# Kernel tuning notes

Hardware: AMD Instinct MI355X
Metric: run time of the kernel (lower is better)

Reference implementation:

```python
import jax, jax.numpy as jnp
import numpy as np

INV_TEMP = 20.0
THRESHOLD = 0.01
SING_CUTOFF = 3.0
D0 = 128  # order-0 descriptor block
EPS = 1e-6


def setup_inputs() -> dict:
    key = jax.random.key(0)
    ks = jax.random.split(key, 6)
    B, N, M, D = 4, 4096, 4096, 256
    K = (D - D0) // 2
    return {
        "keypoints_A": jax.random.uniform(ks[0], (B, N, 2), jnp.float32) * 2.0 - 1.0,
        "descriptions_A": jax.random.normal(ks[1], (B, N, D), jnp.float32),
        "keypoints_B": jax.random.uniform(ks[2], (B, M, 2), jnp.float32) * 2.0 - 1.0,
        "descriptions_B": jax.random.normal(ks[3], (B, M, D), jnp.float32),
        "W_lstsq": jax.random.normal(ks[4], (D0, K), jnp.float32) * 0.1,
        "b_lstsq": jnp.zeros((K,), jnp.float32),
    }


def _svdvals_2x2(A):
    # singular values of [..,2,2] via eigenvalues of A^T A (closed form)
    M = jnp.einsum('...ki,...kj->...ij', A, A)
    t = M[..., 0, 0] + M[..., 1, 1]
    d = M[..., 0, 0] * M[..., 1, 1] - M[..., 0, 1] * M[..., 1, 0]
    disc = jnp.sqrt(jnp.maximum(0.25 * t * t - d, 0.0))
    lam_hi = 0.5 * t + disc
    lam_lo = jnp.maximum(0.5 * t - disc, 0.0)
    return jnp.sqrt(lam_hi), jnp.sqrt(lam_lo)


def reference(keypoints_A, descriptions_A, keypoints_B, descriptions_B, W_lstsq, b_lstsq):
    B, N, D = descriptions_A.shape
    K = (D - D0) // 2
    # --- dual softmax matcher (normalize=True) ---
    dA = descriptions_A / jnp.linalg.norm(descriptions_A, axis=-1, keepdims=True)
    dB = descriptions_B / jnp.linalg.norm(descriptions_B, axis=-1, keepdims=True)
    sim = INV_TEMP * jnp.einsum('bnd,bmd->bnm', dA, dB)  # [B,N,M]
    P = jax.nn.softmax(sim, axis=-2) * jax.nn.softmax(sim, axis=-1)
    # --- mutual nearest neighbors, fixed-shape (one candidate per A-row) ---
    j = jnp.argmax(P, axis=-1)  # [B,N]
    Pij = jnp.take_along_axis(P, j[..., None], axis=-1)[..., 0]
    colmax_j = jnp.take_along_axis(P.max(axis=-2), j, axis=-1)
    valid = (Pij >= colmax_j) & (Pij > THRESHOLD)  # mutual max + threshold
    # --- gather raw descriptors for matched pairs ---
    descB_m = jnp.take_along_axis(descriptions_B, j[..., None], axis=1)  # [B,N,D]
    desc0_A, desc1_A = descriptions_A[..., :D0], descriptions_A[..., D0:]
    desc0_B, desc1_B = descB_m[..., :D0], descB_m[..., D0:]
    # --- lstsq weights from order-0 features ---
    wA = jax.nn.softplus(desc0_A @ W_lstsq + b_lstsq)
    wB = jax.nn.softplus(desc0_B @ W_lstsq + b_lstsq)
    w = jnp.sqrt(wA * wB)  # [B,N,K]
    # --- weighted 2x2 affine lstsq: A x ~ y ---
    X = desc1_A.reshape(B, N, K, 2)
    Y = desc1_B.reshape(B, N, K, 2)
    G = jnp.einsum('bnk,bnki,bnkj->bnij', w, X, X) + EPS * jnp.eye(2, dtype=X.dtype)
    C = jnp.einsum('bnk,bnki,bnkj->bnij', w, Y, X)
    est = jnp.swapaxes(jnp.linalg.solve(G, jnp.swapaxes(C, -1, -2)), -1, -2)  # [B,N,2,2]
    # --- singular value / determinant filter ---
    s_hi, s_lo = _svdvals_2x2(est)
    good = jnp.isfinite(s_hi + s_lo) & (s_hi < SING_CUTOFF) & (s_lo > 1.0 / SING_CUTOFF)
    det = est[..., 0, 0] * est[..., 1, 1] - est[..., 0, 1] * est[..., 1, 0]
    good = good & (det > 0)  # remove_negative_determinants=True
    valid = valid & good
    matches_A = keypoints_A  # row i of A pairs with column j[b,i]
    matches_B = jnp.take_along_axis(keypoints_B, j[..., None], axis=1)
    return matches_A, matches_B, j, valid
```

## Files before the change

kernel.cpp:

```cpp
#include <hip/hip_runtime.h>
#include <math.h>

#define Bb   4
#define Nn   4096
#define Mm   4096
#define Dd   256
#define D0c  128
#define Kc   64

typedef _Float16 half8 __attribute__((ext_vector_type(8)));
typedef float    f32x4 __attribute__((ext_vector_type(4)));

__device__ __forceinline__ unsigned encf(float f) {
    unsigned u = __float_as_uint(f);
    return (u & 0x80000000u) ? ~u : (u | 0x80000000u);
}
__device__ __forceinline__ float decf(unsigned u) {
    return (u & 0x80000000u) ? __uint_as_float(u ^ 0x80000000u) : __uint_as_float(~u);
}
__device__ __forceinline__ float softplusf(float x) {
    return fmaxf(x, 0.f) + log1pf(expf(-fabsf(x)));
}
__device__ __forceinline__ void gl_lds16(const _Float16* g, _Float16* l) {
    __builtin_amdgcn_global_load_lds((const __attribute__((address_space(1))) void*)g,
                                     (__attribute__((address_space(3))) void*)l, 16, 0, 0);
}

__device__ __forceinline__ void decode_tile(int bid, int swz, int& mt, int& nt, int& zz) {
    if (swz == 2) {
        const int xcd = bid & 7, k = bid >> 3;
        zz = xcd >> 2;
        const int s = xcd & 3;
        mt = (s & 1) * 16 + (k & 15);
        nt = (s >> 1) * 16 + (k >> 4);
    } else if (swz == 1) {
        const int xcd = bid & 7, k = bid >> 3;
        zz = 0;
        const int s = xcd >> 1;
        const int t = (xcd & 1) * 128 + k;
        mt = (s & 1) * 16 + (t & 15);
        nt = (s >> 1) * 16 + (t >> 4);
    } else {
        mt = bid & 31; nt = (bid >> 5) & 31; zz = bid >> 10;
    }
}

__global__ __launch_bounds__(256) void prep_kernel(
    const float* __restrict__ dA, const float* __restrict__ dB,
    _Float16* __restrict__ Ah, _Float16* __restrict__ Al,
    _Float16* __restrict__ Bh, _Float16* __restrict__ Bl,
    unsigned* __restrict__ colMaxU)
{
    const int t = threadIdx.x, wave = t >> 6, lane = t & 63;
    const int row = blockIdx.x * 4 + wave;
    if (blockIdx.y == 0 && lane == 0) colMaxU[row] = 0u;
    const float* src = blockIdx.y ? dB : dA;
    _Float16* dh = blockIdx.y ? Bh : Ah;
    _Float16* dl = blockIdx.y ? Bl : Al;
    const float4 v = *(const float4*)&src[(size_t)row * Dd + lane * 4];
    float ss = v.x * v.x + v.y * v.y + v.z * v.z + v.w * v.w;
#pragma unroll
    for (int m = 32; m; m >>= 1) ss += __shfl_xor(ss, m, 64);
    const float inv = 1.0f / sqrtf(ss);
    float x[4] = {v.x * inv, v.y * inv, v.z * inv, v.w * inv};
    union { _Float16 h[4]; uint2 u; } ph, pl;
#pragma unroll
    for (int i = 0; i < 4; i++) {
        _Float16 h = (_Float16)x[i];
        ph.h[i] = h;
        pl.h[i] = (_Float16)((x[i] - (float)h) * 4096.f);
    }
    const size_t toff = (size_t)(row >> 7) * 32768
                      + (size_t)(lane >> 3) * 4096
                      + (size_t)((lane >> 1) & 3) * 1024
                      + (size_t)(row & 127) * 8 + (lane & 1) * 4;
    *(uint2*)&dh[toff] = ph.u;
    *(uint2*)&dl[toff] = pl.u;
}

template<int PB, int STORE>
__global__ __launch_bounds__(256, 2) void sim_kernel(
    const _Float16* __restrict__ Ah, const _Float16* __restrict__ Al,
    const _Float16* __restrict__ Bh, const _Float16* __restrict__ Bl,
    const float* __restrict__ Lrow_g, const float* __restrict__ Lcol_g,
    float* __restrict__ rowsumP, float* __restrict__ colsumP,
    float* __restrict__ rkey, int* __restrict__ rmArr, float* __restrict__ rcvArr,
    unsigned* __restrict__ cmU, float* __restrict__ simG, int b0, int swz)
{
    __shared__ _Float16 lds[2][4][4][128][8];
    __shared__ float    colp[128];
    __shared__ unsigned colu[128];
    __shared__ float    shL[128], shLc[128];

    const int t = threadIdx.x;
    const int wave = t >> 6, lane = t & 63;
    int mt, nt, bbl;
    decode_tile(blockIdx.x, swz, mt, nt, bbl);
    const int bb = b0 + bbl;
    const int n0 = nt * 128, m0 = mt * 128;

    if (PB) {
        if (t < 128) {
            shL[t]  = Lrow_g[bb * Nn + n0 + t];
            shLc[t] = Lcol_g[bb * Mm + m0 + t];
            colu[t] = 0u;
        }
    } else {
        if (t < 128) colp[t] = 0.f;
    }

    const _Float16* gb;
    {
        const size_t offA = (size_t)(bb * Nn + n0) * Dd;
        const size_t offB = (size_t)(bb * Mm + m0) * Dd;
        if      (wave == 0) gb = Ah + offA;
        else if (wave == 1) gb = Al + offA;
        else if (wave == 2) gb = Bh + offB;
        else                gb = Bl + offB;
    }

    f32x4 acc1[2][8], acc2[2][8];
#pragma unroll
    for (int ti = 0; ti < 2; ti++)
#pragma unroll
        for (int tj = 0; tj < 8; tj++) { acc1[ti][tj] = (f32x4)0.f; acc2[ti][tj] = (f32x4)0.f; }

    const int quad = lane >> 4, l15 = lane & 15;
    _Float16* lw0 = &lds[0][wave][0][0][0];
    _Float16* lw1 = &lds[1][wave][0][0][0];

#pragma unroll
    for (int q = 0; q < 8; ++q)
        gl_lds16(gb + q * 512 + lane * 8, lw0 + q * 512);

#pragma unroll
    for (int kc8 = 0; kc8 < 8; ++kc8) {
        const int cur = kc8 & 1;
        if (kc8 < 7) {
            _Float16* nw = cur ? lw0 : lw1;
            const _Float16* gsrc = gb + (kc8 + 1) * 4096;
#pragma unroll
            for (int q = 0; q < 8; ++q)
                gl_lds16(gsrc + q * 512 + lane * 8, nw + q * 512);
            asm volatile("s_waitcnt vmcnt(8)" ::: "memory");
        } else {
            asm volatile("s_waitcnt vmcnt(0)" ::: "memory");
        }
        __builtin_amdgcn_s_barrier();
        __builtin_amdgcn_sched_barrier(0);

        half8 afh[2], afl[2];
        afh[0] = *(const half8*)&lds[cur][0][quad][wave * 32 + l15][0];
        afh[1] = *(const half8*)&lds[cur][0][quad][wave * 32 + 16 + l15][0];
        afl[0] = *(const half8*)&lds[cur][1][quad][wave * 32 + l15][0];
        afl[1] = *(const half8*)&lds[cur][1][quad][wave * 32 + 16 + l15][0];
#pragma unroll
        for (int tj = 0; tj < 8; ++tj) {
            half8 bh = *(const half8*)&lds[cur][2][quad][tj * 16 + l15][0];
            half8 bl = *(const half8*)&lds[cur][3][quad][tj * 16 + l15][0];
#pragma unroll
            for (int ti = 0; ti < 2; ++ti) {
                acc1[ti][tj] = __builtin_amdgcn_mfma_f32_16x16x32_f16(afh[ti], bh, acc1[ti][tj], 0, 0, 0);
                acc2[ti][tj] = __builtin_amdgcn_mfma_f32_16x16x32_f16(afh[ti], bl, acc2[ti][tj], 0, 0, 0);
                acc2[ti][tj] = __builtin_amdgcn_mfma_f32_16x16x32_f16(afl[ti], bh, acc2[ti][tj], 0, 0, 0);
            }
        }
        asm volatile("s_waitcnt lgkmcnt(0)" ::: "memory");
        __builtin_amdgcn_s_barrier();
    }

    if (!PB) {
        float rp[8] = {0.f}, cp[8] = {0.f};
#pragma unroll
        for (int ti = 0; ti < 2; ++ti)
#pragma unroll
            for (int tj = 0; tj < 8; ++tj)
#pragma unroll
                for (int r = 0; r < 4; ++r) {
                    float dot = fmaf(acc2[ti][tj][r], 2.44140625e-4f, acc1[ti][tj][r]);
                    acc1[ti][tj][r] = dot;
                    float e = __expf(fmaf(20.f, dot, -20.f));
                    rp[ti * 4 + r] += e;
                    cp[tj] += e;
                }
#pragma unroll
        for (int i = 0; i < 8; ++i)
#pragma unroll
            for (int m = 1; m < 16; m <<= 1) rp[i] += __shfl_xor(rp[i], m, 64);
        if (l15 == 0) {
#pragma unroll
            for (int ti = 0; ti < 2; ++ti)
#pragma unroll
                for (int r = 0; r < 4; ++r)
                    rowsumP[(size_t)(bb * 32 + mt) * Nn + n0 + wave * 32 + ti * 16 + quad * 4 + r] = rp[ti * 4 + r];
        }
#pragma unroll
        for (int tj = 0; tj < 8; ++tj) {
            cp[tj] += __shfl_xor(cp[tj], 16, 64);
            cp[tj] += __shfl_xor(cp[tj], 32, 64);
        }
        if (quad == 0) {
#pragma unroll
            for (int tj = 0; tj < 8; ++tj) atomicAdd(&colp[tj * 16 + l15], cp[tj]);
        }
        __syncthreads();
        if (t < 128) colsumP[(size_t)(bb * 32 + nt) * Mm + m0 + t] = colp[t];
        if (STORE) {
            float* base = simG + ((size_t)bbl * Nn + n0) * Mm + m0;
#pragma unroll
            for (int ti = 0; ti < 2; ++ti)
#pragma unroll
                for (int r = 0; r < 4; ++r) {
                    float* rowp = base + (size_t)(wave * 32 + ti * 16 + quad * 4 + r) * Mm;
#pragma unroll
                    for (int tj = 0; tj < 8; ++tj)
                        __builtin_nontemporal_store(acc1[ti][tj][r], rowp + tj * 16 + l15);
                }
        }
    } else {
        float Lr[8];
#pragma unroll
        for (int ti = 0; ti < 2; ++ti)
#pragma unroll
            for (int r = 0; r < 4; ++r)
                Lr[ti * 4 + r] = shL[wave * 32 + ti * 16 + quad * 4 + r];

        float bk[8], bc[8];
        int bm[8];
        unsigned cu[8];
#pragma unroll
        for (int i = 0; i < 8; i++) { bk[i] = -INFINITY; bc[i] = -INFINITY; bm[i] = 0x7fffffff; }
#pragma unroll
        for (int j = 0; j < 8; j++) cu[j] = 0u;

#pragma unroll
        for (int ti = 0; ti < 2; ++ti)
#pragma unroll
            for (int tj = 0; tj < 8; ++tj)
#pragma unroll
                for (int r = 0; r < 4; ++r) {
                    float dot = fmaf(acc2[ti][tj][r], 2.44140625e-4f, acc1[ti][tj][r]);
                    float cv = fmaf(40.f, dot, -40.f - Lr[ti * 4 + r]);
                    float kv = cv - shLc[tj * 16 + l15];
                    const int i = ti * 4 + r;
                    if (kv > bk[i]) { bk[i] = kv; bm[i] = m0 + tj * 16 + l15; bc[i] = cv; }
                    unsigned e = encf(cv);
                    if (e > cu[tj]) cu[tj] = e;
                }
#pragma unroll
        for (int i = 0; i < 8; ++i) {
#pragma unroll
            for (int m = 1; m < 16; m <<= 1) {
                float okv = __shfl_xor(bk[i], m, 64);
                int   om  = __shfl_xor(bm[i], m, 64);
                float ocv = __shfl_xor(bc[i], m, 64);
                if (okv > bk[i] || (okv == bk[i] && om < bm[i])) { bk[i] = okv; bm[i] = om; bc[i] = ocv; }
            }
        }
        if (l15 == 0) {
#pragma unroll
            for (int ti = 0; ti < 2; ++ti)
#pragma unroll
                for (int r = 0; r < 4; ++r) {
                    const int i = ti * 4 + r;
                    size_t idx = (size_t)(bb * 32 + mt) * Nn + n0 + wave * 32 + ti * 16 + quad * 4 + r;
                    rkey[idx] = bk[i]; rmArr[idx] = bm[i]; rcvArr[idx] = bc[i];
                }
        }
#pragma unroll
        for (int tj = 0; tj < 8; ++tj) {
            unsigned o = __shfl_xor(cu[tj], 16, 64); if (o > cu[tj]) cu[tj] = o;
            o = __shfl_xor(cu[tj], 32, 64); if (o > cu[tj]) cu[tj] = o;
        }
        if (quad == 0) {
#pragma unroll
            for (int tj = 0; tj < 8; ++tj) atomicMax(&colu[tj * 16 + l15], cu[tj]);
        }
        __syncthreads();
        if (t < 128) cmU[(size_t)(bb * 32 + nt) * Mm + m0 + t] = colu[t];
    }
}

__global__ __launch_bounds__(256) void logsum_kernel(
    const float* __restrict__ rowsumP, const float* __restrict__ colsumP,
    float* __restrict__ Lrow, float* __restrict__ Lcol, int b0, int CB)
{
    int t = blockIdx.x * 256 + threadIdx.x;
    int half = CB * 4096;
    int which = t >= half;
    int idx = which ? (t - half) : t;
    int bb = b0 + (idx >> 12), n = idx & 4095;
    const float* P = which ? colsumP : rowsumP;
    float s = 0.f;
    for (int mt = 0; mt < 32; ++mt) s += P[(size_t)(bb * 32 + mt) * 4096 + n];
    (which ? Lcol : Lrow)[bb * 4096 + n] = logf(s);
}

__global__ __launch_bounds__(256) void scan_kernel(
    const float* __restrict__ simG,
    const float* __restrict__ Lrow, const float* __restrict__ Lcol,
    float* __restrict__ kvP, float* __restrict__ cvP, int* __restrict__ jP,
    unsigned* __restrict__ colMaxU, int b0)
{
    __shared__ unsigned colu[1024];
    const int t = threadIdx.x, wave = t >> 6, lane = t & 63;
    const int blk = blockIdx.x;
    const int bbl = blk >> 9;
    const int r9 = blk & 511;
    const int stripe = r9 >> 2, q = r9 & 3;
    const int bb = b0 + bbl;
    const int col0 = q * 1024;
    const int row0 = stripe * 32 + wave * 8;

    for (int i = t; i < 1024; i += 256) colu[i] = 0u;
    __syncthreads();

    f32x4 Lc4[4], cmax[4];
    const float* LcB = Lcol + bb * Mm + col0;
#pragma unroll
    for (int c = 0; c < 4; ++c) {
        Lc4[c] = *(const f32x4*)&LcB[c * 256 + lane * 4];
        cmax[c] = (f32x4)(-INFINITY);
    }

    const float* rowbase = simG + (size_t)(bbl * Nn + row0) * Mm + col0;
    f32x4 cur[4], nxt[4];
#pragma unroll
    for (int c = 0; c < 4; ++c)
        cur[c] = *(const f32x4*)&rowbase[c * 256 + lane * 4];

    for (int r = 0; r < 8; ++r) {
        if (r < 7) {
            const float* nrow = rowbase + (size_t)(r + 1) * Mm;
#pragma unroll
            for (int c = 0; c < 4; ++c)
                nxt[c] = *(const f32x4*)&nrow[c * 256 + lane * 4];
        }
        const int n = bb * Nn + row0 + r;
        const float Ln = Lrow[n];
        const float cbias = -40.f - Ln;
        float bk = -INFINITY, bc = -INFINITY;
        int bm = 0x7fffffff;
#pragma unroll
        for (int c = 0; c < 4; ++c) {
            float cv0 = fmaf(40.f, cur[c].x, cbias);
            float cv1 = fmaf(40.f, cur[c].y, cbias);
            float cv2 = fmaf(40.f, cur[c].z, cbias);
            float cv3 = fmaf(40.f, cur[c].w, cbias);
            cmax[c].x = fmaxf(cmax[c].x, cv0);
            cmax[c].y = fmaxf(cmax[c].y, cv1);
            cmax[c].z = fmaxf(cmax[c].z, cv2);
            cmax[c].w = fmaxf(cmax[c].w, cv3);
            const int mb = col0 + c * 256 + lane * 4;
            float kv0 = cv0 - Lc4[c].x;
            float kv1 = cv1 - Lc4[c].y;
            float kv2 = cv2 - Lc4[c].z;
            float kv3 = cv3 - Lc4[c].w;
            if (kv0 > bk) { bk = kv0; bm = mb;     bc = cv0; }
            if (kv1 > bk) { bk = kv1; bm = mb + 1; bc = cv1; }
            if (kv2 > bk) { bk = kv2; bm = mb + 2; bc = cv2; }
            if (kv3 > bk) { bk = kv3; bm = mb + 3; bc = cv3; }
        }
#pragma unroll
        for (int sh = 1; sh < 64; sh <<= 1) {
            float okv = __shfl_xor(bk, sh, 64);
            int   om  = __shfl_xor(bm, sh, 64);
            float ocv = __shfl_xor(bc, sh, 64);
            if (okv > bk || (okv == bk && om < bm)) { bk = okv; bm = om; bc = ocv; }
        }
        if (lane == 0) {
            size_t o = ((size_t)bb * Nn + row0 + r) * 4 + q;
            kvP[o] = bk; cvP[o] = bc; jP[o] = bm;
        }
#pragma unroll
        for (int c = 0; c < 4; ++c) cur[c] = nxt[c];
    }
#pragma unroll
    for (int c = 0; c < 4; ++c) {
        const int mb = c * 256 + lane * 4;
        atomicMax(&colu[mb],     encf(cmax[c].x));
        atomicMax(&colu[mb + 1], encf(cmax[c].y));
        atomicMax(&colu[mb + 2], encf(cmax[c].z));
        atomicMax(&colu[mb + 3], encf(cmax[c].w));
    }
    __syncthreads();
    unsigned* cm = colMaxU + (size_t)bb * Mm + col0;
    for (int i = t; i < 1024; i += 256) atomicMax(&cm[i], colu[i]);
}

__global__ __launch_bounds__(256) void validate_kernel(
    const float* __restrict__ kvP, const float* __restrict__ cvP,
    const int* __restrict__ jP, const unsigned* __restrict__ colMaxU,
    float* __restrict__ outJ, int* __restrict__ jIdx, int* __restrict__ v1)
{
    const float LOG_THR = -4.605170185988091f;
    const int p = blockIdx.x * 256 + threadIdx.x;
    const int bb = p >> 12;
    float bk = -INFINITY, bc = -INFINITY;
    int bm = 0x7fffffff;
#pragma unroll
    for (int q = 0; q < 4; ++q) {
        size_t o = (size_t)p * 4 + q;
        float k = kvP[o];
        int   m = jP[o];
        if (k > bk || (k == bk && m < bm)) { bk = k; bm = m; bc = cvP[o]; }
    }
    const float cm = decf(colMaxU[(size_t)bb * Mm + bm]);
    const int ok = (bk > LOG_THR) && (bc >= cm);
    outJ[p] = (float)bm;
    jIdx[p] = bm;
    v1[p] = ok;
}

__global__ __launch_bounds__(256) void finalize_kernel(
    const float* __restrict__ rkey, const int* __restrict__ rmArr,
    const float* __restrict__ rcvArr, const unsigned* __restrict__ cmU,
    float* __restrict__ outJ, int* __restrict__ jIdx, int* __restrict__ v1)
{
    const float LOG_THR = -4.605170185988091f;
    int p = blockIdx.x * 256 + threadIdx.x;
    int bb = p >> 12, n = p & 4095;
    float bk = -INFINITY, bc = -INFINITY;
    int bm = 0;
    for (int mt = 0; mt < 32; ++mt) {
        size_t idx = (size_t)(bb * 32 + mt) * Nn + n;
        float k = rkey[idx];
        if (k > bk) { bk = k; bm = rmArr[idx]; bc = rcvArr[idx]; }
    }
    unsigned u = 0u;
    for (int nt = 0; nt < 32; ++nt) {
        unsigned c = cmU[(size_t)(bb * 32 + nt) * Mm + bm];
        if (c > u) u = c;
    }
    float cm = decf(u);
    int ok = (bk > LOG_THR) && (bc >= cm);
    outJ[p] = (float)bm;
    jIdx[p] = bm;
    v1[p]   = ok;
}

__global__ __launch_bounds__(256) void affine_kernel(
    const float* __restrict__ descA, const float* __restrict__ descB,
    const float* __restrict__ kpA, const float* __restrict__ kpB,
    const float* __restrict__ W, const float* __restrict__ bvec,
    const int* __restrict__ jIdx, const int* __restrict__ v1,
    float* __restrict__ outA, float* __restrict__ outB, float* __restrict__ outV)
{
    __shared__ float Ws[D0c * Kc];
    __shared__ float sbuf[4][4][D0c];
    const int t = threadIdx.x, wave = t >> 6, lane = t & 63;
    for (int i = t; i < D0c * Kc; i += 256) Ws[i] = W[i];
    const float bl = bvec[lane];
    __syncthreads();

    float* s0A = sbuf[wave][0];
    float* s1A = sbuf[wave][1];
    float* s0B = sbuf[wave][2];
    float* s1B = sbuf[wave][3];

    for (int p = 0; p < 8; ++p) {
        const int point = blockIdx.x * 32 + wave * 8 + p;
        const int bb = point >> 12;
        const int j = jIdx[point];
        const float* da = descA + (size_t)point * Dd;
        const float* db = descB + (size_t)(bb * Mm + j) * Dd;
        s0A[lane] = da[lane];       s0A[64 + lane] = da[64 + lane];
        s1A[lane] = da[128 + lane]; s1A[64 + lane] = da[192 + lane];
        s0B[lane] = db[lane];       s0B[64 + lane] = db[64 + lane];
        s1B[lane] = db[128 + lane]; s1B[64 + lane] = db[192 + lane];
        __syncthreads();

        float xa = bl, xb = bl;
#pragma unroll 8
        for (int d = 0; d < 128; ++d) {
            float w_ = Ws[d * 64 + lane];
            xa = fmaf(s0A[d], w_, xa);
            xb = fmaf(s0B[d], w_, xb);
        }
        float wa = softplusf(xa), wb = softplusf(xb);
        float w = sqrtf(wa * wb);
        float x0 = s1A[2 * lane], x1 = s1A[2 * lane + 1];
        float y0 = s1B[2 * lane], y1 = s1B[2 * lane + 1];
        float g00 = w * x0 * x0, g01 = w * x0 * x1, g11 = w * x1 * x1;
        float c00 = w * y0 * x0, c01 = w * y0 * x1;
        float c10 = w * y1 * x0, c11 = w * y1 * x1;
#pragma unroll
        for (int m = 32; m; m >>= 1) {
            g00 += __shfl_xor(g00, m, 64); g01 += __shfl_xor(g01, m, 64); g11 += __shfl_xor(g11, m, 64);
            c00 += __shfl_xor(c00, m, 64); c01 += __shfl_xor(c01, m, 64);
            c10 += __shfl_xor(c10, m, 64); c11 += __shfl_xor(c11, m, 64);
        }
        if (lane == 0) {
            g00 += 1e-6f; g11 += 1e-6f;
            float det = g00 * g11 - g01 * g01;
            float e00 = (c00 * g11 - c01 * g01) / det;
            float e01 = (c01 * g00 - c00 * g01) / det;
            float e10 = (c10 * g11 - c11 * g01) / det;
            float e11 = (c11 * g00 - c10 * g01) / det;
            float m00 = e00 * e00 + e10 * e10;
            float m01 = e00 * e01 + e10 * e11;
            float m11 = e01 * e01 + e11 * e11;
            float tr = m00 + m11;
            float dm = m00 * m11 - m01 * m01;
            float disc = sqrtf(fmaxf(0.25f * tr * tr - dm, 0.f));
            float lhi = 0.5f * tr + disc;
            float llo = fmaxf(0.5f * tr - disc, 0.f);
            float shi = sqrtf(lhi), slo = sqrtf(llo);
            float sdet = e00 * e11 - e01 * e10;
            int good = isfinite(shi + slo) && (shi < 3.0f) && (slo > 0.33333334f) && (sdet > 0.f);
            int valid = v1[point] && good;
            outA[2 * point]     = kpA[2 * point];
            outA[2 * point + 1] = kpA[2 * point + 1];
            const float* kb = kpB + (size_t)(bb * Mm + j) * 2;
            outB[2 * point]     = kb[0];
            outB[2 * point + 1] = kb[1];
            outV[point] = valid ? 1.f : 0.f;
        }
        __syncthreads();
    }
}

extern "C" void kernel_launch(void* const* d_in, const int* in_sizes, int n_in,
                              void* d_out, int out_size, void* d_ws, size_t ws_size,
                              hipStream_t stream) {
    const float* kpA = (const float*)d_in[0];
    const float* dA  = (const float*)d_in[1];
    const float* kpB = (const float*)d_in[2];
    const float* dB  = (const float*)d_in[3];
    const float* W   = (const float*)d_in[4];
    const float* bl  = (const float*)d_in[5];
    float* out = (float*)d_out;

    char* ws = (char*)d_ws;
    _Float16* Ah = (_Float16*)ws;  ws += 8388608;
    _Float16* Al = (_Float16*)ws;  ws += 8388608;
    _Float16* Bh = (_Float16*)ws;  ws += 8388608;
    _Float16* Bl = (_Float16*)ws;  ws += 8388608;
    float*    rowsumP = (float*)ws;    ws += 2097152;
    float*    colsumP = (float*)ws;    ws += 2097152;
    float*    Lrow    = (float*)ws;    ws += 65536;
    float*    Lcol    = (float*)ws;    ws += 65536;
    int*      jIdx    = (int*)ws;      ws += 65536;
    int*      v1      = (int*)ws;      ws += 65536;
    float*    kvP     = (float*)ws;    ws += 262144;
    float*    cvP     = (float*)ws;    ws += 262144;
    int*      jP      = (int*)ws;      ws += 262144;
    unsigned* colMaxU = (unsigned*)ws; ws += 65536;
    char*     big     = ws;

    const size_t base = (size_t)(big - (char*)d_ws);

    float*    rkey  = (float*)big;
    int*      rmArr = (int*)(big + 2097152);
    float*    rcvArr= (float*)(big + 4194304);
    unsigned* cmU   = (unsigned*)(big + 6291456);

    float* outA = out;
    float* outB = out + 32768;
    float* outJ = out + 65536;
    float* outV = out + 81920;

    const size_t per = 67108864ull;
    int CB = 0;
    if      (ws_size >= base + 2 * per) CB = 2;
    else if (ws_size >= base + 1 * per) CB = 1;

    prep_kernel<<<dim3(4096, 2), 256, 0, stream>>>(dA, dB, Ah, Al, Bh, Bl, colMaxU);

    if (CB) {
        float* simG = (float*)big;
        for (int b0 = 0; b0 < Bb; b0 += CB) {
            sim_kernel<0, 1><<<1024 * CB, 256, 0, stream>>>(
                Ah, Al, Bh, Bl, nullptr, nullptr, rowsumP, colsumP,
                nullptr, nullptr, nullptr, nullptr, simG, b0, CB);
            logsum_kernel<<<32 * CB, 256, 0, stream>>>(rowsumP, colsumP, Lrow, Lcol, b0, CB);
            scan_kernel<<<512 * CB, 256, 0, stream>>>(simG, Lrow, Lcol, kvP, cvP, jP, colMaxU, b0);
        }
        validate_kernel<<<64, 256, 0, stream>>>(kvP, cvP, jP, colMaxU, outJ, jIdx, v1);
    } else {
        sim_kernel<0, 0><<<4096, 256, 0, stream>>>(
            Ah, Al, Bh, Bl, nullptr, nullptr, rowsumP, colsumP,
            nullptr, nullptr, nullptr, nullptr, nullptr, 0, 0);
        logsum_kernel<<<32 * Bb, 256, 0, stream>>>(rowsumP, colsumP, Lrow, Lcol, 0, Bb);
        sim_kernel<1, 0><<<4096, 256, 0, stream>>>(
            Ah, Al, Bh, Bl, Lrow, Lcol, nullptr, nullptr,
            rkey, rmArr, rcvArr, cmU, nullptr, 0, 0);
        finalize_kernel<<<64, 256, 0, stream>>>(rkey, rmArr, rcvArr, cmU, outJ, jIdx, v1);
    }
    affine_kernel<<<512, 256, 0, stream>>>(dA, dB, kpA, kpB, W, bl, jIdx, v1, outA, outB, outV);
}
```

Measured before the change: 331.5 us.

## Use 2x2 wave tiling in sim kernel and halve rows per scan block

Changes the per-wave MFMA tile from 32x128 to 64x64 (2x2 wave grid), so each wave does fewer LDS fragment loads per MFMA, since A and B fragments are each reused across four tiles. Row sums and row argmax results from the two column-waves are now merged through shared memory before being written out. Separately, the scan kernel processes 16 rows per block instead of 32, doubling the grid, and uses nontemporal loads for the similarity matrix. This adds extra shared-memory traffic and syncs, raises register count for the 4x4 accumulators, and per-block column max work grows relative to rows.

```diff
diff --git a/kernel.cpp b/kernel.cpp
--- a/kernel.cpp
+++ b/kernel.cpp
@@ -89,11 +89,15 @@
 {
     __shared__ _Float16 lds[2][4][4][128][8];
     __shared__ float    colp[128];
+    __shared__ float    rowp[128];
     __shared__ unsigned colu[128];
     __shared__ float    shL[128], shLc[128];
+    __shared__ float    s_bk[128], s_bc[128];
+    __shared__ int      s_bm[128];
 
     const int t = threadIdx.x;
     const int wave = t >> 6, lane = t & 63;
+    const int wr = wave >> 1, wc = wave & 1;
     int mt, nt, bbl;
     decode_tile(blockIdx.x, swz, mt, nt, bbl);
     const int bb = b0 + bbl;
@@ -106,7 +110,7 @@
             colu[t] = 0u;
         }
     } else {
-        if (t < 128) colp[t] = 0.f;
+        if (t < 128) { colp[t] = 0.f; rowp[t] = 0.f; }
     }
 
     const _Float16* gb;
@@ -119,11 +123,11 @@
         else                gb = Bl + offB;
     }
 
-    f32x4 acc1[2][8], acc2[2][8];
-#pragma unroll
-    for (int ti = 0; ti < 2; ti++)
-#pragma unroll
-        for (int tj = 0; tj < 8; tj++) { acc1[ti][tj] = (f32x4)0.f; acc2[ti][tj] = (f32x4)0.f; }
+    f32x4 acc1[4][4], acc2[4][4];
+#pragma unroll
+    for (int ti = 0; ti < 4; ti++)
+#pragma unroll
+        for (int tj = 0; tj < 4; tj++) { acc1[ti][tj] = (f32x4)0.f; acc2[ti][tj] = (f32x4)0.f; }
 
     const int quad = lane >> 4, l15 = lane & 15;
     _Float16* lw0 = &lds[0][wave][0][0][0];
@@ -149,17 +153,18 @@
         __builtin_amdgcn_s_barrier();
         __builtin_amdgcn_sched_barrier(0);
 
-        half8 afh[2], afl[2];
-        afh[0] = *(const half8*)&lds[cur][0][quad][wave * 32 + l15][0];
-        afh[1] = *(const half8*)&lds[cur][0][quad][wave * 32 + 16 + l15][0];
-        afl[0] = *(const half8*)&lds[cur][1][quad][wave * 32 + l15][0];
-        afl[1] = *(const half8*)&lds[cur][1][quad][wave * 32 + 16 + l15][0];
-#pragma unroll
-        for (int tj = 0; tj < 8; ++tj) {
-            half8 bh = *(const half8*)&lds[cur][2][quad][tj * 16 + l15][0];
-            half8 bl = *(const half8*)&lds[cur][3][quad][tj * 16 + l15][0];
-#pragma unroll
-            for (int ti = 0; ti < 2; ++ti) {
+        half8 afh[4], afl[4];
+#pragma unroll
+        for (int ti = 0; ti < 4; ++ti) {
+            afh[ti] = *(const half8*)&lds[cur][0][quad][wr * 64 + ti * 16 + l15][0];
+            afl[ti] = *(const half8*)&lds[cur][1][quad][wr * 64 + ti * 16 + l15][0];
+        }
+#pragma unroll
+        for (int tj = 0; tj < 4; ++tj) {
+            half8 bh = *(const half8*)&lds[cur][2][quad][wc * 64 + tj * 16 + l15][0];
+            half8 bl = *(const half8*)&lds[cur][3][quad][wc * 64 + tj * 16 + l15][0];
+#pragma unroll
+            for (int ti = 0; ti < 4; ++ti) {
                 acc1[ti][tj] = __builtin_amdgcn_mfma_f32_16x16x32_f16(afh[ti], bh, acc1[ti][tj], 0, 0, 0);
                 acc2[ti][tj] = __builtin_amdgcn_mfma_f32_16x16x32_f16(afh[ti], bl, acc2[ti][tj], 0, 0, 0);
                 acc2[ti][tj] = __builtin_amdgcn_mfma_f32_16x16x32_f16(afl[ti], bh, acc2[ti][tj], 0, 0, 0);
@@ -170,11 +175,11 @@
     }
 
     if (!PB) {
-        float rp[8] = {0.f}, cp[8] = {0.f};
-#pragma unroll
-        for (int ti = 0; ti < 2; ++ti)
-#pragma unroll
-            for (int tj = 0; tj < 8; ++tj)
+        float rp[16] = {0.f}, cp[4] = {0.f};
+#pragma unroll
+        for (int ti = 0; ti < 4; ++ti)
+#pragma unroll
+            for (int tj = 0; tj < 4; ++tj)
 #pragma unroll
                 for (int r = 0; r < 4; ++r) {
                     float dot = fmaf(acc2[ti][tj][r], 2.44140625e-4f, acc1[ti][tj][r]);
@@ -184,71 +189,74 @@
                     cp[tj] += e;
                 }
 #pragma unroll
-        for (int i = 0; i < 8; ++i)
+        for (int i = 0; i < 16; ++i)
 #pragma unroll
             for (int m = 1; m < 16; m <<= 1) rp[i] += __shfl_xor(rp[i], m, 64);
         if (l15 == 0) {
 #pragma unroll
-            for (int ti = 0; ti < 2; ++ti)
+            for (int ti = 0; ti < 4; ++ti)
 #pragma unroll
                 for (int r = 0; r < 4; ++r)
-                    rowsumP[(size_t)(bb * 32 + mt) * Nn + n0 + wave * 32 + ti * 16 + quad * 4 + r] = rp[ti * 4 + r];
-        }
-#pragma unroll
-        for (int tj = 0; tj < 8; ++tj) {
+                    atomicAdd(&rowp[wr * 64 + ti * 16 + quad * 4 + r], rp[ti * 4 + r]);
+        }
+#pragma unroll
+        for (int tj = 0; tj < 4; ++tj) {
             cp[tj] += __shfl_xor(cp[tj], 16, 64);
             cp[tj] += __shfl_xor(cp[tj], 32, 64);
         }
         if (quad == 0) {
 #pragma unroll
-            for (int tj = 0; tj < 8; ++tj) atomicAdd(&colp[tj * 16 + l15], cp[tj]);
+            for (int tj = 0; tj < 4; ++tj) atomicAdd(&colp[wc * 64 + tj * 16 + l15], cp[tj]);
         }
         __syncthreads();
-        if (t < 128) colsumP[(size_t)(bb * 32 + nt) * Mm + m0 + t] = colp[t];
+        if (t < 128) {
+            rowsumP[(size_t)(bb * 32 + mt) * Nn + n0 + t] = rowp[t];
+            colsumP[(size_t)(bb * 32 + nt) * Mm + m0 + t] = colp[t];
+        }
         if (STORE) {
-            float* base = simG + ((size_t)bbl * Nn + n0) * Mm + m0;
-#pragma unroll
-            for (int ti = 0; ti < 2; ++ti)
+            float* base = simG + ((size_t)bbl * Nn + n0) * Mm + m0 + wc * 64;
+#pragma unroll
+            for (int ti = 0; ti < 4; ++ti)
 #pragma unroll
                 for (int r = 0; r < 4; ++r) {
-                    float* rowp = base + (size_t)(wave * 32 + ti * 16 + quad * 4 + r) * Mm;
-#pragma unroll
-                    for (int tj = 0; tj < 8; ++tj)
-                        __builtin_nontemporal_store(acc1[ti][tj][r], rowp + tj * 16 + l15);
+                    float* rowp_ = base + (size_t)(wr * 64 + ti * 16 + quad * 4 + r) * Mm;
+#pragma unroll
+                    for (int tj = 0; tj < 4; ++tj)
+                        __builtin_nontemporal_store(acc1[ti][tj][r], rowp_ + tj * 16 + l15);
                 }
         }
     } else {
-        float Lr[8];
-#pragma unroll
-        for (int ti = 0; ti < 2; ++ti)
+        float Lr[16];
+#pragma unroll
+        for (int ti = 0; ti < 4; ++ti)
 #pragma unroll
             for (int r = 0; r < 4; ++r)
-                Lr[ti * 4 + r] = shL[wave * 32 + ti * 16 + quad * 4 + r];
-
-        float bk[8], bc[8];
-        int bm[8];
-        unsigned cu[8];
-#pragma unroll
-        for (int i = 0; i < 8; i++) { bk[i] = -INFINITY; bc[i] = -INFINITY; bm[i] = 0x7fffffff; }
-#pragma unroll
-        for (int j = 0; j < 8; j++) cu[j] = 0u;
-
-#pragma unroll
-        for (int ti = 0; ti < 2; ++ti)
-#pragma unroll
-            for (int tj = 0; tj < 8; ++tj)
+                Lr[ti * 4 + r] = shL[wr * 64 + ti * 16 + quad * 4 + r];
+
+        float bk[16], bc[16];
+        int bm[16];
+        unsigned cu[4];
+#pragma unroll
+        for (int i = 0; i < 16; i++) { bk[i] = -INFINITY; bc[i] = -INFINITY; bm[i] = 0x7fffffff; }
+#pragma unroll
+        for (int j = 0; j < 4; j++) cu[j] = 0u;
+
+#pragma unroll
+        for (int ti = 0; ti < 4; ++ti)
+#pragma unroll
+            for (int tj = 0; tj < 4; ++tj)
 #pragma unroll
                 for (int r = 0; r < 4; ++r) {
                     float dot = fmaf(acc2[ti][tj][r], 2.44140625e-4f, acc1[ti][tj][r]);
                     float cv = fmaf(40.f, dot, -40.f - Lr[ti * 4 + r]);
-                    float kv = cv - shLc[tj * 16 + l15];
+                    float kv = cv - shLc[wc * 64 + tj * 16 + l15];
                     const int i = ti * 4 + r;
-                    if (kv > bk[i]) { bk[i] = kv; bm[i] = m0 + tj * 16 + l15; bc[i] = cv; }
+                    if (kv > bk[i]) { bk[i] = kv; bm[i] = m0 + wc * 64 + tj * 16 + l15; bc[i] = cv; }
                     unsigned e = encf(cv);
                     if (e > cu[tj]) cu[tj] = e;
                 }
 #pragma unroll
-        for (int i = 0; i < 8; ++i) {
+        for (int i = 0; i < 16; ++i) {
 #pragma unroll
             for (int m = 1; m < 16; m <<= 1) {
                 float okv = __shfl_xor(bk[i], m, 64);
@@ -257,27 +265,43 @@
                 if (okv > bk[i] || (okv == bk[i] && om < bm[i])) { bk[i] = okv; bm[i] = om; bc[i] = ocv; }
             }
         }
-        if (l15 == 0) {
-#pragma unroll
-            for (int ti = 0; ti < 2; ++ti)
+        if (l15 == 0 && wc == 0) {
+#pragma unroll
+            for (int ti = 0; ti < 4; ++ti)
 #pragma unroll
                 for (int r = 0; r < 4; ++r) {
-                    const int i = ti * 4 + r;
-                    size_t idx = (size_t)(bb * 32 + mt) * Nn + n0 + wave * 32 + ti * 16 + quad * 4 + r;
-                    rkey[idx] = bk[i]; rmArr[idx] = bm[i]; rcvArr[idx] = bc[i];
+                    const int row = wr * 64 + ti * 16 + quad * 4 + r, i = ti * 4 + r;
+                    s_bk[row] = bk[i]; s_bm[row] = bm[i]; s_bc[row] = bc[i];
                 }
         }
-#pragma unroll
-        for (int tj = 0; tj < 8; ++tj) {
+        __syncthreads();
+        if (l15 == 0 && wc == 1) {
+#pragma unroll
+            for (int ti = 0; ti < 4; ++ti)
+#pragma unroll
+                for (int r = 0; r < 4; ++r) {
+                    const int row = wr * 64 + ti * 16 + quad * 4 + r, i = ti * 4 + r;
+                    float k0 = s_bk[row];
+                    if (bk[i] > k0 || (bk[i] == k0 && bm[i] < s_bm[row])) {
+                        s_bk[row] = bk[i]; s_bm[row] = bm[i]; s_bc[row] = bc[i];
+                    }
+                }
+        }
+#pragma unroll
+        for (int tj = 0; tj < 4; ++tj) {
             unsigned o = __shfl_xor(cu[tj], 16, 64); if (o > cu[tj]) cu[tj] = o;
             o = __shfl_xor(cu[tj], 32, 64); if (o > cu[tj]) cu[tj] = o;
         }
         if (quad == 0) {
 #pragma unroll
-            for (int tj = 0; tj < 8; ++tj) atomicMax(&colu[tj * 16 + l15], cu[tj]);
+            for (int tj = 0; tj < 4; ++tj) atomicMax(&colu[wc * 64 + tj * 16 + l15], cu[tj]);
         }
         __syncthreads();
-        if (t < 128) cmU[(size_t)(bb * 32 + nt) * Mm + m0 + t] = colu[t];
+        if (t < 128) {
+            size_t idx = (size_t)(bb * 32 + mt) * Nn + n0 + t;
+            rkey[idx] = s_bk[t]; rmArr[idx] = s_bm[t]; rcvArr[idx] = s_bc[t];
+            cmU[(size_t)(bb * 32 + nt) * Mm + m0 + t] = colu[t];
+        }
     }
 }
 
@@ -305,12 +329,12 @@
     __shared__ unsigned colu[1024];
     const int t = threadIdx.x, wave = t >> 6, lane = t & 63;
     const int blk = blockIdx.x;
-    const int bbl = blk >> 9;
-    const int r9 = blk & 511;
-    const int stripe = r9 >> 2, q = r9 & 3;
+    const int bbl = blk >> 10;
+    const int r10 = blk & 1023;
+    const int stripe = r10 >> 2, q = r10 & 3;
     const int bb = b0 + bbl;
     const int col0 = q * 1024;
-    const int row0 = stripe * 32 + wave * 8;
+    const int row0 = stripe * 16 + wave * 4;
 
     for (int i = t; i < 1024; i += 256) colu[i] = 0u;
     __syncthreads();
@@ -327,14 +351,14 @@
     f32x4 cur[4], nxt[4];
 #pragma unroll
     for (int c = 0; c < 4; ++c)
-        cur[c] = *(const f32x4*)&rowbase[c * 256 + lane * 4];
-
-    for (int r = 0; r < 8; ++r) {
-        if (r < 7) {
+        cur[c] = __builtin_nontemporal_load((const f32x4*)&rowbase[c * 256 + lane * 4]);
+
+    for (int r = 0; r < 4; ++r) {
+        if (r < 3) {
             const float* nrow = rowbase + (size_t)(r + 1) * Mm;
 #pragma unroll
             for (int c = 0; c < 4; ++c)
-                nxt[c] = *(const f32x4*)&nrow[c * 256 + lane * 4];
+                nxt[c] = __builtin_nontemporal_load((const f32x4*)&nrow[c * 256 + lane * 4]);
         }
         const int n = bb * Nn + row0 + r;
         const float Ln = Lrow[n];
@@ -574,7 +598,7 @@
                 Ah, Al, Bh, Bl, nullptr, nullptr, rowsumP, colsumP,
                 nullptr, nullptr, nullptr, nullptr, simG, b0, CB);
             logsum_kernel<<<32 * CB, 256, 0, stream>>>(rowsumP, colsumP, Lrow, Lcol, b0, CB);
-            scan_kernel<<<512 * CB, 256, 0, stream>>>(simG, Lrow, Lcol, kvP, cvP, jP, colMaxU, b0);
+            scan_kernel<<<1024 * CB, 256, 0, stream>>>(simG, Lrow, Lcol, kvP, cvP, jP, colMaxU, b0);
         }
         validate_kernel<<<64, 256, 0, stream>>>(kvP, cvP, jP, colMaxU, outJ, jIdx, v1);
     } else {
```

Result: faster. 316.4 us (-4.5%).
